# Optimization experiments

Measured on AMD Instinct MI355X. Metric: run time of the kernel, lower is better.

The kernel has to match this reference:

```python
import jax, jax.numpy as jnp
import numpy as np

# Grid constants from init_kwargs: output_shape = [1, 10, 200, 176, 64]
D, H, W, C = 10, 200, 176, 64
N_VOX = 30000


def _conv_block(x, w, scale, bias, stride, pad):
    # x: [N,C,D,H,W]; w: [O,I,kd,kh,kw]; ZeroPad3d then valid Conv3d,
    # then fused (inference) BatchNorm3d + ReLU.
    x = jnp.pad(x, ((0, 0), (0, 0), (pad[0], pad[0]), (pad[1], pad[1]), (pad[2], pad[2])))
    x = jax.lax.conv_general_dilated(
        x, w, window_strides=stride, padding='VALID',
        dimension_numbers=('NCDHW', 'OIDHW', 'NCDHW'))
    s = scale[None, :, None, None, None]
    b = bias[None, :, None, None, None]
    return jax.nn.relu(x * s + b)


def setup_inputs() -> dict:
    key = jax.random.key(0)
    kf, kd, kh, kw, k1, k2, k3, ks = jax.random.split(key, 8)
    voxel_features = jax.random.normal(kf, (N_VOX, C), dtype=jnp.float32)
    # coors columns: (batch_idx, d, h, w) each in range
    b_idx = jnp.zeros((N_VOX,), dtype=jnp.int32)  # batch_size = 1
    d_idx = jax.random.randint(kd, (N_VOX,), 0, D, dtype=jnp.int32)
    h_idx = jax.random.randint(kh, (N_VOX,), 0, H, dtype=jnp.int32)
    w_idx = jax.random.randint(kw, (N_VOX,), 0, W, dtype=jnp.int32)
    coors = jnp.stack([b_idx, d_idx, h_idx, w_idx], axis=1)
    fan = 1.0 / np.sqrt(C * 27)
    W1 = jax.random.normal(k1, (64, C, 3, 3, 3), dtype=jnp.float32) * fan
    W2 = jax.random.normal(k2, (64, 64, 3, 3, 3), dtype=jnp.float32) * fan
    W3 = jax.random.normal(k3, (64, 64, 3, 3, 3), dtype=jnp.float32) * fan
    ks1, ks2, ks3 = jax.random.split(ks, 3)
    scale1 = jax.random.uniform(ks1, (64,), dtype=jnp.float32, minval=0.5, maxval=1.5)
    scale2 = jax.random.uniform(ks2, (64,), dtype=jnp.float32, minval=0.5, maxval=1.5)
    scale3 = jax.random.uniform(ks3, (64,), dtype=jnp.float32, minval=0.5, maxval=1.5)
    bias1 = jax.random.normal(jax.random.fold_in(ks1, 1), (64,), dtype=jnp.float32) * 0.1
    bias2 = jax.random.normal(jax.random.fold_in(ks2, 1), (64,), dtype=jnp.float32) * 0.1
    bias3 = jax.random.normal(jax.random.fold_in(ks3, 1), (64,), dtype=jnp.float32) * 0.1
    return {
        'voxel_features': voxel_features, 'coors': coors, 'batch_size': 1,
        'W1': W1, 'scale1': scale1, 'bias1': bias1,
        'W2': W2, 'scale2': scale2, 'bias2': bias2,
        'W3': W3, 'scale3': scale3, 'bias3': bias3,
    }


def reference(voxel_features, coors, batch_size,
              W1, scale1, bias1, W2, scale2, bias2, W3, scale3, bias3):
    # scatter_nd: sparse voxel features -> dense [B, D, H, W, C]
    dense = jnp.zeros((batch_size, D, H, W, C), dtype=voxel_features.dtype)
    dense = dense.at[coors[:, 0], coors[:, 1], coors[:, 2], coors[:, 3]].set(voxel_features)
    x = dense.transpose(0, 4, 1, 2, 3)  # [B, C, D, H, W]
    # middle_conv: Pad(1)+Conv3d s=(2,1,1); Pad(0,1,1)+Conv3d s=1; Pad(1)+Conv3d s=(2,1,1)
    x = _conv_block(x, W1, scale1, bias1, (2, 1, 1), (1, 1, 1))   # D: 10 -> 5
    x = _conv_block(x, W2, scale2, bias2, (1, 1, 1), (0, 1, 1))   # D: 5 -> 3
    x = _conv_block(x, W3, scale3, bias3, (2, 1, 1), (1, 1, 1))   # D: 3 -> 2
    N, Cc, Dd, Hh, Ww = x.shape
    return x.reshape(N, Cc * Dd, Hh, Ww)  # [B, 128, H, W]
```

## Files before the change

kernel.cpp:

```cpp
#include <hip/hip_runtime.h>
#include <cstddef>

#define HH 200
#define WW 176
#define HP 202
#define WP 178
#define D_IN 10
#define D1 5
#define D2 3
#define D3 2
#define SLICE ((size_t)HP * WP * 64)

#define LBALL_BYTES (9 * 8192)

typedef _Float16 h8 __attribute__((ext_vector_type(8)));
typedef float f4 __attribute__((ext_vector_type(4)));

__device__ __forceinline__ void gl_lds16(const void* g, void* l) {
    __builtin_amdgcn_global_load_lds(
        (const __attribute__((address_space(1))) void*)g,
        (__attribute__((address_space(3))) void*)l, 16, 0, 0);
}

__global__ __launch_bounds__(256) void prep_k(const float* __restrict__ W1,
                                              const float* __restrict__ W2,
                                              const float* __restrict__ W3,
                                              _Float16* __restrict__ wdst,
                                              _Float16* __restrict__ A2,
                                              _Float16* __restrict__ A3,
                                              const int* __restrict__ coors,
                                              int* __restrict__ winner, int nvox) {
    const int b = blockIdx.x;
    if (b < 8) {
        _Float16* base = (b < D1) ? (A2 + (size_t)b * SLICE) : (A3 + (size_t)(b - D1) * SLICE);
        const h8 z = {};
        for (int t = threadIdx.x; t < 6080; t += 256) {
            size_t off;
            if (t < 2848) {
                int r = t / 1424, c = t - r * 1424;
                off = (size_t)(r ? (HP - 1) : 0) * WP * 64 + (size_t)c * 8;
            } else {
                int u = t - 2848;
                int c = u / 1616, v = u - c * 1616;
                int hr = v >> 3, o = v & 7;
                off = ((size_t)hr * WP + (c ? (WP - 1) : 0)) * 64 + (size_t)o * 8;
            }
            *(h8*)(base + off) = z;
        }
    } else if (b < 8 + 1296) {
        int idx = (b - 8) * 256 + threadIdx.x;
        if (idx < 3 * 27 * 64 * 64) {
            int set = idx / 110592;
            int r = idx - set * 110592;
            const float* src = set == 0 ? W1 : (set == 1 ? W2 : W3);
            int ci = r & 63;
            int co = (r >> 6) & 63;
            int tap = r >> 12;
            int s = ci >> 3, j = ci & 7;
            wdst[set * 110592 + tap * 4096 + co * 64 + (((s ^ (co & 7)) << 3) | j)] =
                (_Float16)src[(co * 64 + ci) * 27 + tap];
        }
    } else {
        int v = (b - 1304) * 256 + threadIdx.x;
        if (v < nvox) {
            int d = coors[v * 4 + 1], h = coors[v * 4 + 2], w = coors[v * 4 + 3];
            atomicMax(&winner[(d * HH + h) * WW + w], v + 1);
        }
    }
}

__global__ __launch_bounds__(256) void scatter_k(const float* __restrict__ feat,
                                                 const int* __restrict__ coors,
                                                 const int* __restrict__ winner,
                                                 _Float16* __restrict__ A, int nvox) {
    int v = blockIdx.x * 4 + (threadIdx.x >> 6);
    int ci = threadIdx.x & 63;
    if (v >= nvox) return;
    int d = coors[v * 4 + 1], h = coors[v * 4 + 2], w = coors[v * 4 + 3];
    if (winner[(d * HH + h) * WW + w] != v + 1) return;
    int P = w + 1;
    int swz = (((ci >> 3) ^ (P & 7)) << 3) | (ci & 7);
    A[(size_t)d * SLICE + ((size_t)(h + 1) * WP + P) * 64 + swz] = (_Float16)feat[v * 64 + ci];
}

template <int FINAL, int RPW>
__global__ __launch_bounds__(256, 1) void conv_mfma_k(
    const _Float16* __restrict__ in, void* __restrict__ outp,
    const _Float16* __restrict__ wt,
    const float* __restrict__ scale, const float* __restrict__ bias,
    int inD, int strideD, int padD) {
    constexpr int BROWS = 4 * RPW;
    constexpr int AR = BROWS + 2;
    constexpr int NSTG = (AR * 400 + 63) / 64;
    constexpr int LA = NSTG * 1024;
    constexpr int CMAX = AR * 400 - 1;

    __shared__ char smem_raw[LA + LBALL_BYTES];
    _Float16* la = (_Float16*)smem_raw;
    char* lball = smem_raw + LA;

    const int lane = threadIdx.x & 63;
    const int wave = threadIdx.x >> 6;
    const int l16 = lane & 15;
    const int quad = lane >> 4;
    const int h0 = blockIdx.y * BROWS;
    const int wb = blockIdx.x * 48;
    const int d = blockIdx.z;

    int kd_lo = padD - d * strideD; if (kd_lo < 0) kd_lo = 0;
    int kd_hi = inD - 1 - d * strideD + padD; if (kd_hi > 2) kd_hi = 2;

    f4 acc[RPW][3][4];
#pragma unroll
    for (int rr = 0; rr < RPW; ++rr)
#pragma unroll
        for (int mt = 0; mt < 3; ++mt)
#pragma unroll
            for (int nt = 0; nt < 4; ++nt) acc[rr][mt][nt] = (f4){0.f, 0.f, 0.f, 0.f};

    for (int kd = kd_lo; kd <= kd_hi; ++kd) {
        const int zd = d * strideD + kd - padD;
        const _Float16* __restrict__ aplane = in + (size_t)zd * SLICE;
        const _Float16* __restrict__ wkd = wt + (size_t)kd * 9 * 4096;

        for (int j = wave; j < NSTG; j += 4) {
            int c = j * 64 + lane;
            if (c > CMAX) c = CMAX;
            int r = c / 400;
            int rem = c - r * 400;
            int px = rem >> 3, s = rem & 7;
            int g = wb + px; if (g > 177) g = 177;
            gl_lds16(aplane + ((size_t)(h0 + r) * WP + g) * 64 + s * 8,
                     smem_raw + j * 1024);
        }
#pragma unroll
        for (int i = 0; i < 18; ++i) {
            int k = i * 4 + wave;
            gl_lds16(wkd + (size_t)k * 512 + (size_t)lane * 8, lball + k * 1024);
        }
        asm volatile("s_waitcnt vmcnt(0)" ::: "memory");
        __builtin_amdgcn_sched_barrier(0);
        __builtin_amdgcn_s_barrier();
        __builtin_amdgcn_sched_barrier(0);

        __builtin_amdgcn_s_setprio(1);
#pragma unroll
        for (int t = 0; t < 9; ++t) {
            const int kh = t / 3;
            const int kw = t - 3 * kh;
            const _Float16* lb = (const _Float16*)(lball + t * 8192);
#pragma unroll
            for (int ch = 0; ch < 2; ++ch) {
                const int q = ch * 4 + quad;
                h8 b[4];
#pragma unroll
                for (int nt = 0; nt < 4; ++nt)
                    b[nt] = *(const h8*)(lb + (nt * 16 + l16) * 64 +
                                         ((q ^ (l16 & 7)) << 3));
#pragma unroll
                for (int rr = 0; rr < RPW; ++rr) {
                    const int row = wave * RPW + rr + kh;
#pragma unroll
                    for (int mt = 0; mt < 3; ++mt) {
                        const int px = mt * 16 + l16 + kw;
                        h8 a = *(const h8*)(la + ((size_t)row * 50 + px) * 64 +
                                            ((q ^ (px & 7)) << 3));
#pragma unroll
                        for (int nt = 0; nt < 4; ++nt)
                            acc[rr][mt][nt] = __builtin_amdgcn_mfma_f32_16x16x32_f16(
                                a, b[nt], acc[rr][mt][nt], 0, 0, 0);
                    }
                }
            }
        }
        __builtin_amdgcn_s_setprio(0);
        asm volatile("s_waitcnt lgkmcnt(0)" ::: "memory");
        __builtin_amdgcn_sched_barrier(0);
        __builtin_amdgcn_s_barrier();
        __builtin_amdgcn_sched_barrier(0);
    }

    if (FINAL) {
#pragma unroll
        for (int nt = 0; nt < 4; ++nt) {
            const int co = nt * 16 + l16;
            const float s = scale[co];
            const float bb = bias[co];
#pragma unroll
            for (int rr = 0; rr < RPW; ++rr) {
                const int h = h0 + wave * RPW + rr;
#pragma unroll
                for (int mt = 0; mt < 3; ++mt) {
                    const int w0 = wb + mt * 16 + quad * 4;
                    if (w0 < WW) {
                        f4 v;
#pragma unroll
                        for (int r = 0; r < 4; ++r) {
                            float x = acc[rr][mt][nt][r] * s + bb;
                            v[r] = x > 0.f ? x : 0.f;
                        }
                        *(f4*)((float*)outp + (((size_t)(co * 2 + d)) * HH + h) * WW + w0) = v;
                    }
                }
            }
        }
    } else {
        _Float16* epb = (_Float16*)smem_raw;
#pragma unroll
        for (int nt = 0; nt < 4; ++nt) {
            const int co = nt * 16 + l16;
            const float s = scale[co];
            const float bb = bias[co];
#pragma unroll
            for (int rr = 0; rr < RPW; ++rr) {
                _Float16* ep = epb + (size_t)(wave * RPW + rr) * (48 * 72);
#pragma unroll
                for (int mt = 0; mt < 3; ++mt) {
#pragma unroll
                    for (int r = 0; r < 4; ++r) {
                        float x = acc[rr][mt][nt][r] * s + bb;
                        x = x > 0.f ? x : 0.f;
                        ep[(mt * 16 + quad * 4 + r) * 72 + co] = (_Float16)x;
                    }
                }
            }
        }
        __builtin_amdgcn_s_barrier();
        const int lim = (WW - wb) * 8;
#pragma unroll
        for (int rr = 0; rr < RPW; ++rr) {
            const int h = h0 + wave * RPW + rr;
            const _Float16* ep = epb + (size_t)(wave * RPW + rr) * (48 * 72);
#pragma unroll
            for (int cv = 0; cv < 6; ++cv) {
                if (cv * 64 < lim) {
                    const int c2 = cv * 64 + lane;
                    const int pxl = c2 >> 3, s = c2 & 7;
                    h8 v = *(const h8*)(ep + pxl * 72 + s * 8);
                    const int P = wb + pxl + 1;
                    *(h8*)((_Float16*)outp + (size_t)d * SLICE +
                           ((size_t)(h + 1) * WP + P) * 64 + ((s ^ (P & 7)) << 3)) = v;
                }
            }
        }
    }
}

extern "C" void kernel_launch(void* const* d_in, const int* in_sizes, int n_in,
                              void* d_out, int out_size, void* d_ws, size_t ws_size,
                              hipStream_t stream) {
    const float* feat   = (const float*)d_in[0];
    const int*   coors  = (const int*)d_in[1];
    const float* W1     = (const float*)d_in[3];
    const float* scale1 = (const float*)d_in[4];
    const float* bias1  = (const float*)d_in[5];
    const float* W2     = (const float*)d_in[6];
    const float* scale2 = (const float*)d_in[7];
    const float* bias2  = (const float*)d_in[8];
    const float* W3     = (const float*)d_in[9];
    const float* scale3 = (const float*)d_in[10];
    const float* bias3  = (const float*)d_in[11];
    const int nvox = in_sizes[0] / 64;

    const size_t nA1 = (size_t)D_IN * SLICE;
    const size_t nWin = (size_t)D_IN * HH * WW;
    const size_t nA2 = (size_t)D1 * SLICE;
    const size_t nA3 = (size_t)D2 * SLICE;
    const size_t nWT = (size_t)27 * 64 * 64;

    _Float16* A1 = (_Float16*)d_ws;
    int* win = (int*)(A1 + nA1);
    _Float16* A2 = (_Float16*)(win + nWin);
    _Float16* A3 = A2 + nA2;
    _Float16* wt1 = A3 + nA3;
    _Float16* wt2 = wt1 + nWT;
    _Float16* wt3 = wt2 + nWT;

    hipMemsetAsync(d_ws, 0, nA1 * sizeof(_Float16) + nWin * sizeof(int), stream);

    const int win_blk = (nvox + 255) / 256;
    prep_k<<<8 + 1296 + win_blk, 256, 0, stream>>>(W1, W2, W3, wt1, A2, A3,
                                                   coors, win, nvox);
    scatter_k<<<(nvox + 3) / 4, 256, 0, stream>>>(feat, coors, win, A1, nvox);

    dim3 blk(256);
    conv_mfma_k<0, 2><<<dim3(4, 25, D1), blk, 0, stream>>>(A1, A2, wt1, scale1, bias1, D_IN, 2, 1);
    conv_mfma_k<0, 1><<<dim3(4, 50, D2), blk, 0, stream>>>(A2, A3, wt2, scale2, bias2, D1, 1, 0);
    conv_mfma_k<1, 1><<<dim3(4, 50, D3), blk, 0, stream>>>(A3, (float*)d_out, wt3, scale3, bias3, D2, 2, 1);
}
```

Baseline: 221.4 us.

## Read conv weights directly from global, reuse A fragments across kh, raise occupancy

Drops the per-kd staging of all 9 weight taps into LDS. B fragments are now loaded straight from global/L2 using a new tap/ci-chunk-major weight layout. The tap loop is restructured over kw so each wave loads RPW+2 rows of A fragments once and reuses them across the three kh taps. Launch bounds go from 1 to 2 blocks per CU, since the smaller LDS footprint allows it. This risks more global-load latency inside the MFMA loop and more register pressure from holding the ag and b arrays. It also removes an epilogue barrier before the LDS staging read-back, which may race because waves read rows written by other lanes.

```diff
diff --git a/kernel.cpp b/kernel.cpp
--- a/kernel.cpp
+++ b/kernel.cpp
@@ -10,8 +10,6 @@
 #define D2 3
 #define D3 2
 #define SLICE ((size_t)HP * WP * 64)
-
-#define LBALL_BYTES (9 * 8192)
 
 typedef _Float16 h8 __attribute__((ext_vector_type(8)));
 typedef float f4 __attribute__((ext_vector_type(4)));
@@ -56,8 +54,7 @@
             int ci = r & 63;
             int co = (r >> 6) & 63;
             int tap = r >> 12;
-            int s = ci >> 3, j = ci & 7;
-            wdst[set * 110592 + tap * 4096 + co * 64 + (((s ^ (co & 7)) << 3) | j)] =
+            wdst[set * 110592 + tap * 4096 + (ci >> 3) * 512 + co * 8 + (ci & 7)] =
                 (_Float16)src[(co * 64 + ci) * 27 + tap];
         }
     } else {
@@ -84,7 +81,7 @@
 }
 
 template <int FINAL, int RPW>
-__global__ __launch_bounds__(256, 1) void conv_mfma_k(
+__global__ __launch_bounds__(256, 2) void conv_mfma_k(
     const _Float16* __restrict__ in, void* __restrict__ outp,
     const _Float16* __restrict__ wt,
     const float* __restrict__ scale, const float* __restrict__ bias,
@@ -95,9 +92,8 @@
     constexpr int LA = NSTG * 1024;
     constexpr int CMAX = AR * 400 - 1;
 
-    __shared__ char smem_raw[LA + LBALL_BYTES];
+    __shared__ char smem_raw[LA];
     _Float16* la = (_Float16*)smem_raw;
-    char* lball = smem_raw + LA;
 
     const int lane = threadIdx.x & 63;
     const int wave = threadIdx.x >> 6;
@@ -133,11 +129,6 @@
             gl_lds16(aplane + ((size_t)(h0 + r) * WP + g) * 64 + s * 8,
                      smem_raw + j * 1024);
         }
-#pragma unroll
-        for (int i = 0; i < 18; ++i) {
-            int k = i * 4 + wave;
-            gl_lds16(wkd + (size_t)k * 512 + (size_t)lane * 8, lball + k * 1024);
-        }
         asm volatile("s_waitcnt vmcnt(0)" ::: "memory");
         __builtin_amdgcn_sched_barrier(0);
         __builtin_amdgcn_s_barrier();
@@ -145,32 +136,57 @@
 
         __builtin_amdgcn_s_setprio(1);
 #pragma unroll
-        for (int t = 0; t < 9; ++t) {
-            const int kh = t / 3;
-            const int kw = t - 3 * kh;
-            const _Float16* lb = (const _Float16*)(lball + t * 8192);
+        for (int kw = 0; kw < 3; ++kw) {
 #pragma unroll
             for (int ch = 0; ch < 2; ++ch) {
                 const int q = ch * 4 + quad;
-                h8 b[4];
+                h8 b[3][4];
 #pragma unroll
                 for (int nt = 0; nt < 4; ++nt)
-                    b[nt] = *(const h8*)(lb + (nt * 16 + l16) * 64 +
-                                         ((q ^ (l16 & 7)) << 3));
-#pragma unroll
-                for (int rr = 0; rr < RPW; ++rr) {
-                    const int row = wave * RPW + rr + kh;
+                    b[0][nt] = *(const h8*)(wkd + (size_t)kw * 4096 + (q << 9) +
+                                            ((nt * 16 + l16) << 3));
+                h8 ag[RPW + 2][3];
+#pragma unroll
+                for (int r = 0; r < RPW + 2; ++r)
 #pragma unroll
                     for (int mt = 0; mt < 3; ++mt) {
                         const int px = mt * 16 + l16 + kw;
-                        h8 a = *(const h8*)(la + ((size_t)row * 50 + px) * 64 +
-                                            ((q ^ (px & 7)) << 3));
+                        ag[r][mt] = *(const h8*)(la +
+                            ((size_t)(wave * RPW + r) * 50 + px) * 64 +
+                            ((q ^ (px & 7)) << 3));
+                    }
+#pragma unroll
+                for (int nt = 0; nt < 4; ++nt)
+                    b[1][nt] = *(const h8*)(wkd + (size_t)(3 + kw) * 4096 + (q << 9) +
+                                            ((nt * 16 + l16) << 3));
+#pragma unroll
+                for (int rr = 0; rr < RPW; ++rr)
+#pragma unroll
+                    for (int mt = 0; mt < 3; ++mt)
 #pragma unroll
                         for (int nt = 0; nt < 4; ++nt)
                             acc[rr][mt][nt] = __builtin_amdgcn_mfma_f32_16x16x32_f16(
-                                a, b[nt], acc[rr][mt][nt], 0, 0, 0);
-                    }
-                }
+                                ag[rr][mt], b[0][nt], acc[rr][mt][nt], 0, 0, 0);
+#pragma unroll
+                for (int nt = 0; nt < 4; ++nt)
+                    b[2][nt] = *(const h8*)(wkd + (size_t)(6 + kw) * 4096 + (q << 9) +
+                                            ((nt * 16 + l16) << 3));
+#pragma unroll
+                for (int rr = 0; rr < RPW; ++rr)
+#pragma unroll
+                    for (int mt = 0; mt < 3; ++mt)
+#pragma unroll
+                        for (int nt = 0; nt < 4; ++nt)
+                            acc[rr][mt][nt] = __builtin_amdgcn_mfma_f32_16x16x32_f16(
+                                ag[rr + 1][mt], b[1][nt], acc[rr][mt][nt], 0, 0, 0);
+#pragma unroll
+                for (int rr = 0; rr < RPW; ++rr)
+#pragma unroll
+                    for (int mt = 0; mt < 3; ++mt)
+#pragma unroll
+                        for (int nt = 0; nt < 4; ++nt)
+                            acc[rr][mt][nt] = __builtin_amdgcn_mfma_f32_16x16x32_f16(
+                                ag[rr + 2][mt], b[2][nt], acc[rr][mt][nt], 0, 0, 0);
             }
         }
         __builtin_amdgcn_s_setprio(0);
@@ -225,7 +241,6 @@
                 }
             }
         }
-        __builtin_amdgcn_s_barrier();
         const int lim = (WW - wb) * 8;
 #pragma unroll
         for (int rr = 0; rr < RPW; ++rr) {
```

Measured after the change: 187.2 us. 15.5% less time.
